# Optimization experiments

Hardware: AMD Instinct MI355X
Metric: run time of the kernel (lower is better)

## Reference

```python
import jax, jax.numpy as jnp
import numpy as np

TEMP = 1.0
POOL_K = 0.5
BN_EPS = 1e-5
B, N, D = 16, 256, 128


def setup_inputs() -> dict:
    key = jax.random.key(0)
    ks = jax.random.split(key, 8)
    s = 0.05
    return {
        "x": jax.random.normal(ks[0], (B, N, D), jnp.float32),
        "att_proj_w": jax.random.normal(ks[1], (D, D), jnp.float32) * s,
        "att_proj_b": jnp.zeros((D,), jnp.float32),
        "att_weight": jax.random.normal(ks[2], (D, 1), jnp.float32) * s,
        "pwa_w": jax.random.normal(ks[3], (D, D), jnp.float32) * s,
        "pwa_b": jnp.zeros((D,), jnp.float32),
        "pwoa_w": jax.random.normal(ks[4], (D, D), jnp.float32) * s,
        "pwoa_b": jnp.zeros((D,), jnp.float32),
        "bn_gamma": jnp.ones((D,), jnp.float32),
        "bn_beta": jnp.zeros((D,), jnp.float32),
        "bn_mean": jnp.zeros((D,), jnp.float32),
        "bn_var": jnp.ones((D,), jnp.float32),
        "pool_w": jax.random.normal(ks[5], (D, 1), jnp.float32) * s,
        "pool_b": jnp.zeros((1,), jnp.float32),
    }


def reference(x, att_proj_w, att_proj_b, att_weight, pwa_w, pwa_b,
              pwoa_w, pwoa_b, bn_gamma, bn_beta, bn_mean, bn_var,
              pool_w, pool_b):
    # ---- GraphAttentionLayer (eval mode: dropout = identity) ----
    # pairwise node outer product: (B, N, N, D)
    pair = x[:, :, None, :] * x[:, None, :, :]
    # att_proj + tanh, then project to scalar per node pair
    a = jnp.tanh(pair @ att_proj_w + att_proj_b)          # (B,N,N,D)
    logits = (a @ att_weight)[..., 0] / TEMP              # (B,N,N)
    # softmax over dim=-2 (the first node axis of the (N,N) map)
    att = jax.nn.softmax(logits, axis=1)                  # (B,N,N)
    # project: att_map @ x through proj_with_att, plus skip branch
    agg = jnp.einsum("bij,bjd->bid", att, x)              # (B,N,D)
    h = (agg @ pwa_w + pwa_b) + (x @ pwoa_w + pwoa_b)
    # BatchNorm1d in eval mode over feature dim
    h = (h - bn_mean) * jax.lax.rsqrt(bn_var + BN_EPS) * bn_gamma + bn_beta
    h = jax.nn.selu(h)
    # ---- GraphPool (eval mode: dropout = identity) ----
    scores = jax.nn.sigmoid(h @ pool_w + pool_b)          # (B,N,1)
    k_nodes = max(int(N * POOL_K), 1)
    _, idx = jax.lax.top_k(scores[..., 0], k_nodes)       # (B,k)
    hs = h * scores                                       # (B,N,D)
    out = jnp.take_along_axis(hs, idx[:, :, None], axis=1)  # (B,k,D)
    return out
```

## Files before the change

### kernel.cpp

```cpp
#include <hip/hip_runtime.h>
#include <math.h>

typedef float f32x4 __attribute__((ext_vector_type(4)));
typedef short s16x8 __attribute__((ext_vector_type(8)));

#define L2E 1.4426950408889634f
#define C2L2E 2.885390081777927f

__global__ void k0_prep(const float* __restrict__ W,
                        unsigned short* __restrict__ gWhi,
                        unsigned short* __restrict__ gWlo,
                        float* __restrict__ S) {
  int bid = blockIdx.x;
  if (bid < 64) {
    int t = bid * 256 + threadIdx.x;
    int d = t >> 7, e = t & 127;
    float w = W[d * 128 + e];
    unsigned u = __float_as_uint(w);
    unsigned hb = (u + 0x7fffu + ((u >> 16) & 1u)) >> 16;
    float r = w - __uint_as_float(hb << 16);
    unsigned ul = __float_as_uint(r);
    unsigned lb = (ul + 0x7fffu + ((ul >> 16) & 1u)) >> 16;
    int addr = e * 128 + (d ^ ((e & 7) << 3));
    gWhi[addr] = (unsigned short)hb;
    gWlo[addr] = (unsigned short)lb;
  } else {
    S[(bid - 64) * 256 + threadIdx.x] = 0.f;
  }
}

__global__ __launch_bounds__(512, 4) void kA_logits(
    const float* __restrict__ x, const unsigned short* __restrict__ gWhi,
    const unsigned short* __restrict__ gWlo, const float* __restrict__ apb,
    const float* __restrict__ av, float* __restrict__ Lg,
    float* __restrict__ S) {
  __shared__ __align__(16) unsigned short sWhi[16384];
  __shared__ __align__(16) unsigned short sWlo[16384];
  __shared__ __align__(16) float sXj[16 * 132];
  __shared__ float sRow[16][8];
  __shared__ float sMir[16];

  int tt = blockIdx.x, ti = 0;
  while (tt >= 16 - ti) { tt -= 16 - ti; ++ti; }
  const int tj = ti + tt;
  const int b = blockIdx.y;
  const int i0 = ti * 16, j0 = tj * 16;
  const int tid = threadIdx.x;

  {
    const uint4* shi = (const uint4*)gWhi;
    const uint4* slo = (const uint4*)gWlo;
    uint4* dhi = (uint4*)sWhi;
    uint4* dlo = (uint4*)sWlo;
#pragma unroll
    for (int r = 0; r < 4; ++r) {
      dhi[tid + 512 * r] = shi[tid + 512 * r];
      dlo[tid + 512 * r] = slo[tid + 512 * r];
    }
    const float4* xsrc = (const float4*)(x + ((size_t)(b * 256 + j0)) * 128);
    *(float4*)&sXj[(tid >> 5) * 132 + (tid & 31) * 4] = xsrc[tid];
  }
  __syncthreads();

  const int lane = tid & 63;
  const int w = tid >> 6;
  const int quad = lane >> 4;
  const int col = lane & 15;
  const int swz = (col & 7) << 3;

  float vw[8];
  f32x4 acc[2][8];
#pragma unroll
  for (int et = 0; et < 8; ++et) {
    float bi = apb[col + 16 * et];
    vw[et] = av[col + 16 * et];
#pragma unroll
    for (int mt = 0; mt < 2; ++mt) acc[mt][et] = (f32x4){bi, bi, bi, bi};
  }

  const float* xib = x + ((size_t)(b * 256 + i0 + 2 * w)) * 128;

#pragma unroll
  for (int kstep = 0; kstep < 4; ++kstep) {
    const int k0 = kstep * 32 + quad * 8;
    float4 xj0 = *(const float4*)&sXj[col * 132 + k0];
    float4 xj1 = *(const float4*)&sXj[col * 132 + k0 + 4];
    s16x8 Ah[2], Al[2];
#pragma unroll
    for (int mt = 0; mt < 2; ++mt) {
      const float* xip = xib + mt * 128 + k0;
      float4 xi0 = *(const float4*)xip;
      float4 xi1 = *(const float4*)(xip + 4);
      float pv[8];
      pv[0] = xi0.x * xj0.x; pv[1] = xi0.y * xj0.y;
      pv[2] = xi0.z * xj0.z; pv[3] = xi0.w * xj0.w;
      pv[4] = xi1.x * xj1.x; pv[5] = xi1.y * xj1.y;
      pv[6] = xi1.z * xj1.z; pv[7] = xi1.w * xj1.w;
      uint4 hp, lp;
      unsigned* hq = (unsigned*)&hp;
      unsigned* lq = (unsigned*)&lp;
#pragma unroll
      for (int p = 0; p < 4; ++p) {
        unsigned u0 = __float_as_uint(pv[2 * p]);
        unsigned u1 = __float_as_uint(pv[2 * p + 1]);
        hq[p] = __builtin_amdgcn_perm(u1, u0, 0x07060302);
        float h0 = __uint_as_float(u0 & 0xffff0000u);
        float h1 = __uint_as_float(u1 & 0xffff0000u);
        unsigned v0 = __float_as_uint(pv[2 * p] - h0) + 0x8000u;
        unsigned v1 = __float_as_uint(pv[2 * p + 1] - h1) + 0x8000u;
        lq[p] = __builtin_amdgcn_perm(v1, v0, 0x07060302);
      }
      Ah[mt] = *(s16x8*)&hp;
      Al[mt] = *(s16x8*)&lp;
    }
#pragma unroll
    for (int et = 0; et < 8; ++et) {
      const int addr = (col + 16 * et) * 128 + (k0 ^ swz);
      s16x8 bh = *(const s16x8*)&sWhi[addr];
      s16x8 bl = *(const s16x8*)&sWlo[addr];
#pragma unroll
      for (int mt = 0; mt < 2; ++mt) {
        acc[mt][et] = __builtin_amdgcn_mfma_f32_16x16x32_bf16(Ah[mt], bh, acc[mt][et], 0, 0, 0);
        acc[mt][et] = __builtin_amdgcn_mfma_f32_16x16x32_bf16(Al[mt], bh, acc[mt][et], 0, 0, 0);
        acc[mt][et] = __builtin_amdgcn_mfma_f32_16x16x32_bf16(Ah[mt], bl, acc[mt][et], 0, 0, 0);
      }
    }
  }

  float E[2];
#pragma unroll
  for (int mt = 0; mt < 2; ++mt) {
    float ls[4] = {0.f, 0.f, 0.f, 0.f};
#pragma unroll
    for (int et = 0; et < 8; ++et) {
#pragma unroll
      for (int r = 0; r < 4; ++r) {
        float e2 = __builtin_amdgcn_exp2f(acc[mt][et][r] * C2L2E);
        float t = 1.0f - 2.0f * __builtin_amdgcn_rcpf(e2 + 1.0f);
        ls[r] += t * vw[et];
      }
    }
#pragma unroll
    for (int m = 1; m < 16; m <<= 1) {
      ls[0] += __shfl_xor(ls[0], m);
      ls[1] += __shfl_xor(ls[1], m);
      ls[2] += __shfl_xor(ls[2], m);
      ls[3] += __shfl_xor(ls[3], m);
    }
    float fl = (col == 0) ? ls[0] : (col == 1) ? ls[1] : (col == 2) ? ls[2] : ls[3];
    E[mt] = __builtin_amdgcn_exp2f(fl * L2E);
  }

  if (col < 4) {
    const int j = j0 + quad * 4 + col;
    float2 val = {E[0], E[1]};
    *(float2*)&Lg[((size_t)(b * 256 + j)) * 256 + i0 + 2 * w] = val;
    sRow[quad * 4 + col][w] = E[0] + E[1];
  }

  if (ti != tj) {
    if (col < 4) {
      const int j = j0 + quad * 4 + col;
#pragma unroll
      for (int mt = 0; mt < 2; ++mt)
        Lg[((size_t)(b * 256 + i0 + 2 * w + mt)) * 256 + j] = E[mt];
    }
#pragma unroll
    for (int mt = 0; mt < 2; ++mt) {
      float v = (col < 4) ? E[mt] : 0.f;
#pragma unroll
      for (int m = 1; m < 64; m <<= 1) v += __shfl_xor(v, m);
      if (lane == 0) sMir[2 * w + mt] = v;
    }
  }
  __syncthreads();
  if (tid < 16) {
    float rs = sRow[tid][0];
#pragma unroll
    for (int q = 1; q < 8; ++q) rs += sRow[tid][q];
    atomicAdd(&S[b * 256 + j0 + tid], rs);
    if (ti != tj) atomicAdd(&S[b * 256 + i0 + tid], sMir[tid]);
  }
}

__global__ void kB_aggh(const float* __restrict__ Lg, const float* __restrict__ S,
                        const float* __restrict__ x,
                        const float* __restrict__ pwa, const float* __restrict__ pwoa,
                        const float* __restrict__ pwab, const float* __restrict__ pwob,
                        const float* __restrict__ gam, const float* __restrict__ bet,
                        const float* __restrict__ mea, const float* __restrict__ varr,
                        const float* __restrict__ plw, const float* __restrict__ plb,
                        float* __restrict__ h, float* __restrict__ scores) {
  const int b = blockIdx.y, i0 = blockIdx.x * 8;
  const int tid = threadIdx.x;
  const int il = tid >> 5, dl = tid & 31;
  __shared__ float sInv[256];
  __shared__ float satt[16][8];
  __shared__ float sxj[2048];
  __shared__ float sa[1024];
  __shared__ float sxi[1024];
  __shared__ double sScD[8][32];

  sInv[tid] = 1.0f / S[b * 256 + tid];
  ((float4*)sxi)[tid] = ((const float4*)(x + ((size_t)(b * 256 + i0)) * 128))[tid];

  float acc[4] = {0.f, 0.f, 0.f, 0.f};
  for (int jj = 0; jj < 256; jj += 16) {
    __syncthreads();
    if (tid < 128)
      satt[tid >> 3][tid & 7] =
          Lg[((size_t)(b * 256 + jj + (tid >> 3))) * 256 + i0 + (tid & 7)] *
          sInv[jj + (tid >> 3)];
    const float4* xsrc = (const float4*)(x + ((size_t)(b * 256 + jj)) * 128);
    ((float4*)sxj)[tid] = xsrc[tid];
    ((float4*)sxj)[tid + 256] = xsrc[tid + 256];
    __syncthreads();
#pragma unroll
    for (int jl = 0; jl < 16; ++jl) {
      float a = satt[jl][il];
      float4 xv = *(const float4*)&sxj[jl * 128 + dl * 4];
      acc[0] += a * xv.x; acc[1] += a * xv.y;
      acc[2] += a * xv.z; acc[3] += a * xv.w;
    }
  }
  __syncthreads();
  *(float4*)&sa[il * 128 + dl * 4] = *(float4*)acc;
  __syncthreads();

  double z[4] = {0, 0, 0, 0};
  for (int k = 0; k < 128; ++k) {
    double a = (double)sa[il * 128 + k];
    float4 wv = *(const float4*)(pwa + k * 128 + dl * 4);
    z[0] += a * (double)wv.x; z[1] += a * (double)wv.y;
    z[2] += a * (double)wv.z; z[3] += a * (double)wv.w;
  }
  for (int k = 0; k < 128; ++k) {
    double a = (double)sxi[il * 128 + k];
    float4 wv = *(const float4*)(pwoa + k * 128 + dl * 4);
    z[0] += a * (double)wv.x; z[1] += a * (double)wv.y;
    z[2] += a * (double)wv.z; z[3] += a * (double)wv.w;
  }
  float o[4];
#pragma unroll
  for (int q = 0; q < 4; ++q) {
    int d = dl * 4 + q;
    double hv = z[q] + (double)pwab[d] + (double)pwob[d];
    double bn = (hv - (double)mea[d]) * (1.0 / sqrt((double)varr[d] + 1e-5)) *
                    (double)gam[d] +
                (double)bet[d];
    float bf = (float)bn;
    o[q] = bf > 0.f ? 1.0507009873554805f * bf
                    : 1.7580993408473766f *
                          (__builtin_amdgcn_exp2f(bf * L2E) - 1.0f);
  }
  *(float4*)(h + ((size_t)(b * 256 + i0 + il)) * 128 + dl * 4) = *(float4*)o;

  sScD[il][dl] = (double)o[0] * (double)plw[dl * 4] +
                 (double)o[1] * (double)plw[dl * 4 + 1] +
                 (double)o[2] * (double)plw[dl * 4 + 2] +
                 (double)o[3] * (double)plw[dl * 4 + 3];
  __syncthreads();
  if (tid < 8) {
    double zz = (double)plb[0];
    for (int c = 0; c < 32; ++c) zz += sScD[tid][c];
    scores[b * 256 + i0 + tid] = (float)(1.0 / (1.0 + exp(-zz)));
  }
}

__global__ __launch_bounds__(1024) void kC_topk(const float* __restrict__ h,
                                                const float* __restrict__ scores,
                                                float* __restrict__ out) {
  const int b = blockIdx.x, tid = threadIdx.x;
  const int t = tid >> 2, c = tid & 3;
  __shared__ float sc[256];
  __shared__ int ipart[256][4];
  __shared__ int sel[128];

  if (c == 0) sc[t] = scores[b * 256 + t];
  __syncthreads();
  {
    const float st = sc[t];
    int r = 0;
    for (int m = c * 64; m < c * 64 + 64; ++m) {
      float sm = sc[m];
      r += (sm > st) || (sm == st && m < t);
    }
    ipart[t][c] = r;
  }
  __syncthreads();
  if (c == 0) {
    int rank = ipart[t][0] + ipart[t][1] + ipart[t][2] + ipart[t][3];
    if (rank < 128) sel[rank] = t;
  }
  __syncthreads();
  const float4* h4 = (const float4*)(h + (size_t)b * 256 * 128);
  float4* o4 = (float4*)(out + (size_t)b * 128 * 128);
#pragma unroll
  for (int r = 0; r < 4; ++r) {
    int v = tid + 1024 * r;
    int row = v >> 5, q = v & 31;
    int src = sel[row];
    float ss = sc[src];
    float4 hv = h4[src * 32 + q];
    float4 ov;
    ov.x = hv.x * ss; ov.y = hv.y * ss; ov.z = hv.z * ss; ov.w = hv.w * ss;
    o4[row * 32 + q] = ov;
  }
}

extern "C" void kernel_launch(void* const* d_in, const int* in_sizes, int n_in,
                              void* d_out, int out_size, void* d_ws, size_t ws_size,
                              hipStream_t stream) {
  const float* x    = (const float*)d_in[0];
  const float* apw  = (const float*)d_in[1];
  const float* apb  = (const float*)d_in[2];
  const float* av   = (const float*)d_in[3];
  const float* pwa  = (const float*)d_in[4];
  const float* pwab = (const float*)d_in[5];
  const float* pwoa = (const float*)d_in[6];
  const float* pwob = (const float*)d_in[7];
  const float* gam  = (const float*)d_in[8];
  const float* bet  = (const float*)d_in[9];
  const float* mea  = (const float*)d_in[10];
  const float* varr = (const float*)d_in[11];
  const float* plw  = (const float*)d_in[12];
  const float* plb  = (const float*)d_in[13];
  float* out = (float*)d_out;

  unsigned short* gWhi = (unsigned short*)d_ws;
  unsigned short* gWlo = gWhi + 16384;
  float* S  = (float*)((char*)d_ws + 65536);
  float* Lg = (float*)((char*)d_ws + 81920);
  float* hb = Lg + (size_t)16 * 256 * 256;
  float* sco = hb + (size_t)16 * 256 * 128;

  k0_prep<<<80, 256, 0, stream>>>(apw, gWhi, gWlo, S);
  kA_logits<<<dim3(136, 16), 512, 0, stream>>>(x, gWhi, gWlo, apb, av, Lg, S);
  kB_aggh<<<dim3(32, 16), 256, 0, stream>>>(Lg, S, x, pwa, pwoa, pwab, pwob,
                                            gam, bet, mea, varr, plw, plb, hb, sco);
  kC_topk<<<16, 1024, 0, stream>>>(hb, sco, out);
}
```

Baseline: 182.7 us.

## Stream attention-projection weights through double-buffered K-slices to cut LDS and raise occupancy

The bf16 hi/lo weight matrices are re-laid out in global memory as four 32-wide K-slices with a new XOR swizzle. The logits kernel now keeps only two slices in shared memory and prefetches the next slice into registers while the current slice's MFMAs run, then stores it and syncs. This shrinks shared memory per block from about 64KB to about 16KB, and the launch-bounds occupancy hint goes from 4 to 6. In exchange it adds three extra block barriers per tile and more global weight loads spread through the loop.

```diff
diff --git a/kernel.cpp b/kernel.cpp
--- a/kernel.cpp
+++ b/kernel.cpp
@@ -21,7 +21,8 @@
     float r = w - __uint_as_float(hb << 16);
     unsigned ul = __float_as_uint(r);
     unsigned lb = (ul + 0x7fffu + ((ul >> 16) & 1u)) >> 16;
-    int addr = e * 128 + (d ^ ((e & 7) << 3));
+    int s = d >> 5, kl = d & 31;
+    int addr = s * 4096 + e * 32 + (kl ^ (((e >> 1) & 3) << 3));
     gWhi[addr] = (unsigned short)hb;
     gWlo[addr] = (unsigned short)lb;
   } else {
@@ -29,13 +30,13 @@
   }
 }
 
-__global__ __launch_bounds__(512, 4) void kA_logits(
+__global__ __launch_bounds__(512, 6) void kA_logits(
     const float* __restrict__ x, const unsigned short* __restrict__ gWhi,
     const unsigned short* __restrict__ gWlo, const float* __restrict__ apb,
     const float* __restrict__ av, float* __restrict__ Lg,
     float* __restrict__ S) {
-  __shared__ __align__(16) unsigned short sWhi[16384];
-  __shared__ __align__(16) unsigned short sWlo[16384];
+  __shared__ __align__(16) unsigned short sWhi[2][4096];
+  __shared__ __align__(16) unsigned short sWlo[2][4096];
   __shared__ __align__(16) float sXj[16 * 132];
   __shared__ float sRow[16][8];
   __shared__ float sMir[16];
@@ -48,15 +49,8 @@
   const int tid = threadIdx.x;
 
   {
-    const uint4* shi = (const uint4*)gWhi;
-    const uint4* slo = (const uint4*)gWlo;
-    uint4* dhi = (uint4*)sWhi;
-    uint4* dlo = (uint4*)sWlo;
-#pragma unroll
-    for (int r = 0; r < 4; ++r) {
-      dhi[tid + 512 * r] = shi[tid + 512 * r];
-      dlo[tid + 512 * r] = slo[tid + 512 * r];
-    }
+    ((uint4*)sWhi[0])[tid] = ((const uint4*)gWhi)[tid];
+    ((uint4*)sWlo[0])[tid] = ((const uint4*)gWlo)[tid];
     const float4* xsrc = (const float4*)(x + ((size_t)(b * 256 + j0)) * 128);
     *(float4*)&sXj[(tid >> 5) * 132 + (tid & 31) * 4] = xsrc[tid];
   }
@@ -66,7 +60,7 @@
   const int w = tid >> 6;
   const int quad = lane >> 4;
   const int col = lane & 15;
-  const int swz = (col & 7) << 3;
+  const int xsw = ((col >> 1) & 3) << 3;
 
   float vw[8];
   f32x4 acc[2][8];
@@ -82,6 +76,13 @@
 
 #pragma unroll
   for (int kstep = 0; kstep < 4; ++kstep) {
+    const int cb = kstep & 1;
+    uint4 rh, rl;
+    if (kstep < 3) {
+      rh = ((const uint4*)(gWhi + (kstep + 1) * 4096))[tid];
+      rl = ((const uint4*)(gWlo + (kstep + 1) * 4096))[tid];
+    }
+
     const int k0 = kstep * 32 + quad * 8;
     float4 xj0 = *(const float4*)&sXj[col * 132 + k0];
     float4 xj1 = *(const float4*)&sXj[col * 132 + k0 + 4];
@@ -113,17 +114,24 @@
       Ah[mt] = *(s16x8*)&hp;
       Al[mt] = *(s16x8*)&lp;
     }
+    const int kq = (quad * 8) ^ xsw;
 #pragma unroll
     for (int et = 0; et < 8; ++et) {
-      const int addr = (col + 16 * et) * 128 + (k0 ^ swz);
-      s16x8 bh = *(const s16x8*)&sWhi[addr];
-      s16x8 bl = *(const s16x8*)&sWlo[addr];
+      const int addr = (col + 16 * et) * 32 + kq;
+      s16x8 bh = *(const s16x8*)&sWhi[cb][addr];
+      s16x8 bl = *(const s16x8*)&sWlo[cb][addr];
 #pragma unroll
       for (int mt = 0; mt < 2; ++mt) {
         acc[mt][et] = __builtin_amdgcn_mfma_f32_16x16x32_bf16(Ah[mt], bh, acc[mt][et], 0, 0, 0);
         acc[mt][et] = __builtin_amdgcn_mfma_f32_16x16x32_bf16(Al[mt], bh, acc[mt][et], 0, 0, 0);
         acc[mt][et] = __builtin_amdgcn_mfma_f32_16x16x32_bf16(Ah[mt], bl, acc[mt][et], 0, 0, 0);
       }
+    }
+    if (kstep < 3) {
+      const int nb = cb ^ 1;
+      ((uint4*)sWhi[nb])[tid] = rh;
+      ((uint4*)sWlo[nb])[tid] = rl;
+      __syncthreads();
     }
   }
 
```

After: 430.2 us. 135% more time.
